# Kernel optimization log

Hardware: AMD Instinct MI355X
Metric: run time of the kernel (lower is better)

## Reference

```python
import jax, jax.numpy as jnp
import numpy as np

D_MODEL = 512
N_HEADS = 8
EDGE_FEAT_DIM = 4
NUM_GRAPHS = 64
NODES_PER_GRAPH = 128
N_NODES = NUM_GRAPHS * NODES_PER_GRAPH          # 8192
EDGES_PER_GRAPH = 4096                           # avg degree 32
N_EDGES = NUM_GRAPHS * EDGES_PER_GRAPH           # 262144


def setup_inputs() -> dict:
    key = jax.random.key(0)
    ks = jax.random.split(key, 12)
    s = 0.02
    x = jax.random.normal(ks[0], (N_NODES, D_MODEL), jnp.float32)
    # edges constrained within their graph (block-diagonal structure)
    g_of_e = jnp.arange(N_EDGES, dtype=jnp.int32) // EDGES_PER_GRAPH
    src = g_of_e * NODES_PER_GRAPH + jax.random.randint(ks[1], (N_EDGES,), 0, NODES_PER_GRAPH, jnp.int32)
    dst = g_of_e * NODES_PER_GRAPH + jax.random.randint(ks[2], (N_EDGES,), 0, NODES_PER_GRAPH, jnp.int32)
    edge_index = jnp.stack([src, dst]).astype(jnp.int32)
    edge_attr = jax.random.normal(ks[3], (N_EDGES, EDGE_FEAT_DIM), jnp.float32)
    batch = jnp.repeat(jnp.arange(NUM_GRAPHS, dtype=jnp.int32), NODES_PER_GRAPH)
    # projection weights (in,out) convention: y = x @ W + b
    Wq = jax.random.normal(ks[4], (D_MODEL, D_MODEL), jnp.float32) * s
    Wk = jax.random.normal(ks[5], (D_MODEL, D_MODEL), jnp.float32) * s
    Wv = jax.random.normal(ks[6], (D_MODEL, D_MODEL), jnp.float32) * s
    Wo = jax.random.normal(ks[7], (D_MODEL, D_MODEL), jnp.float32) * s
    bq = jnp.zeros((D_MODEL,), jnp.float32)
    bk = jnp.zeros((D_MODEL,), jnp.float32)
    bv = jnp.zeros((D_MODEL,), jnp.float32)
    bo = jnp.zeros((D_MODEL,), jnp.float32)
    # edge bias MLP: edge_feat_dim -> d_model -> n_heads
    W1 = jax.random.normal(ks[8], (EDGE_FEAT_DIM, D_MODEL), jnp.float32) * s
    b1 = jnp.zeros((D_MODEL,), jnp.float32)
    W2 = jax.random.normal(ks[9], (D_MODEL, N_HEADS), jnp.float32) * s
    b2 = jnp.zeros((N_HEADS,), jnp.float32)
    return {"x": x, "edge_index": edge_index, "edge_attr": edge_attr, "batch": batch,
            "n_g": NODES_PER_GRAPH,
            "Wq": Wq, "bq": bq, "Wk": Wk, "bk": bk, "Wv": Wv, "bv": bv,
            "Wo": Wo, "bo": bo, "W1": W1, "b1": b1, "W2": W2, "b2": b2}


def reference(x, edge_index, edge_attr, batch, n_g, Wq, bq, Wk, bk, Wv, bv, Wo, bo, W1, b1, W2, b2):
    # batch is contiguous equal-size blocks of n_g nodes per graph, so the
    # per-graph Python loop of the original collapses to a batched (G, n_g)
    # block-diagonal attention. Dropout is identity (eval / p used only in train).
    N, d_model = x.shape
    H = W2.shape[1]
    d_k = d_model // H
    G = N // n_g
    scale = 1.0 / float(np.sqrt(d_k))

    Q = (x @ Wq + bq).reshape(G, n_g, H, d_k)
    K = (x @ Wk + bk).reshape(G, n_g, H, d_k)
    V = (x @ Wv + bv).reshape(G, n_g, H, d_k)

    # (G, i, j, h) dense per-graph scores
    scores = jnp.einsum('gihd,gjhd->gijh', Q, K) * scale

    # edge bias: MLP(edge_attr) -> (E, H), scattered at (graph, local_src, local_dst)
    bias = jax.nn.relu(edge_attr @ W1 + b1) @ W2 + b2
    ge = edge_index[0] // n_g
    ls = edge_index[0] % n_g
    ld = edge_index[1] % n_g
    scores = scores.at[ge, ls, ld].add(bias)

    attn = jax.nn.softmax(scores, axis=2)  # softmax over j (keys), matches dim=1 of (i,j,h)
    out = jnp.einsum('gijh,gjhd->gihd', attn, V).reshape(N, d_model)
    return out @ Wo + bo
```

## Files before the change

### kernel.cpp

```cpp
#include <hip/hip_runtime.h>
#include <hip/hip_bf16.h>

#define E_TOTAL 262144
#define NG      128
#define GRAPHS  64
#define NHEADS  8
#define DKH     64
#define DMODEL  512
#define NNODES  8192

typedef __bf16 bf16x8 __attribute__((ext_vector_type(8)));
typedef float  f32x4  __attribute__((ext_vector_type(4)));
typedef short  s16x4  __attribute__((ext_vector_type(4)));
typedef unsigned short u16x8 __attribute__((ext_vector_type(8)));

typedef __attribute__((address_space(3))) char lds_char;
typedef const __attribute__((address_space(1))) char glb_char;

__device__ inline __hip_bfloat16 f2hbf(float f) { return __float2bfloat16(f); }
__device__ inline unsigned short f2u16(float f) {
    return __builtin_bit_cast(unsigned short, __float2bfloat16(f));
}
__device__ inline __bf16 f2bf(float f) {
    return __builtin_bit_cast(__bf16, f2u16(f));
}

__global__ __launch_bounds__(256) void prep_kernel(
    const float* __restrict__ x, __hip_bfloat16* __restrict__ xb,
    const float* __restrict__ Wq, const float* __restrict__ Wk,
    const float* __restrict__ Wv, const float* __restrict__ Wo,
    const float* __restrict__ W1, const float* __restrict__ b1,
    const float* __restrict__ W2, const float* __restrict__ b2,
    __hip_bfloat16* __restrict__ wqkvt, __hip_bfloat16* __restrict__ wot,
    __hip_bfloat16* __restrict__ w1fragt, float* __restrict__ b1f,
    __hip_bfloat16* __restrict__ w2at, float* __restrict__ b2f)
{
    int blk0 = blockIdx.x, tid = threadIdx.x;
    if (blk0 < 4096) {
        int idx = (blk0 * 256 + tid) * 4;
        float4 v = *(const float4*)(x + idx);
        ushort4 o;
        o.x = f2u16(v.x); o.y = f2u16(v.y); o.z = f2u16(v.z); o.w = f2u16(v.w);
        *(ushort4*)((unsigned short*)xb + idx) = o;
        return;
    }
    int blk = blk0 - 4096;
    if (blk < 256) {
        __shared__ __align__(16) __hip_bfloat16 tile[64][65];
        const float* src;
        __hip_bfloat16* dstT;
        int n0, k0, nb;
        if (blk < 192) {
            int nt = blk % 24, ktile = blk / 24;
            n0 = nt * 64; k0 = ktile * 64;
            if (n0 < 512)       { src = Wq; nb = n0; }
            else if (n0 < 1024) { src = Wk; nb = n0 - 512; }
            else                { src = Wv; nb = n0 - 1024; }
            dstT = wqkvt;
        } else {
            int t = blk - 192;
            n0 = (t % 8) * 64; k0 = (t / 8) * 64; nb = n0;
            src = Wo; dstT = wot;
        }
        #pragma unroll
        for (int i = 0; i < 16; ++i) {
            int idx = tid + i * 256;
            int kr = idx >> 6, nc = idx & 63;
            tile[kr][nc] = f2hbf(src[(size_t)(k0 + kr) * 512 + nb + nc]);
        }
        __syncthreads();
        #pragma unroll
        for (int i = 0; i < 16; ++i) {
            int idx = tid + i * 256;
            int nr = idx >> 6, kc = idx & 63;
            dstT[(size_t)(n0 + nr) * 512 + k0 + kc] = tile[kc][nr];
        }
    } else {
        __hip_bfloat16 z = f2hbf(0.f);
        for (int n = tid; n < 512; n += 256) {
            #pragma unroll
            for (int j = 0; j < 4; ++j) w1fragt[n * 8 + j] = f2hbf(W1[(size_t)j * 512 + n]);
            #pragma unroll
            for (int j = 4; j < 8; ++j) w1fragt[n * 8 + j] = z;
        }
        for (int i = tid; i < 512; i += 256) b1f[i] = b1[i];
        for (int i = tid; i < 32 * 64 * 4; i += 256) {
            int t = i >> 8, lane = (i >> 2) & 63, j = i & 3;
            int q = lane >> 4, l = lane & 15;
            w2at[i] = (l < 8) ? f2hbf(W2[(size_t)(16 * t + 4 * q + j) * 8 + l]) : z;
        }
        if (tid < 8) b2f[tid] = b2[tid];
    }
}

__device__ __forceinline__ void gemm_body(
    const __hip_bfloat16* __restrict__ A, const __hip_bfloat16* __restrict__ BT,
    int mode, int row0, int col0,
    const float* __restrict__ bq, const float* __restrict__ bk,
    const float* __restrict__ bv,
    __hip_bfloat16* __restrict__ qkv, __hip_bfloat16* __restrict__ vt,
    const float* __restrict__ bo, float* __restrict__ out,
    __hip_bfloat16* As, __hip_bfloat16* Bs)
{
    const int K = 512;
    int tid = threadIdx.x;
    int lane = tid & 63, quad = lane >> 4, l16 = lane & 15;
    int wave = tid >> 6, wi = wave >> 1, wj = wave & 1;

    f32x4 acc[4][4];
    #pragma unroll
    for (int a = 0; a < 4; a++)
        #pragma unroll
        for (int b = 0; b < 4; b++)
            #pragma unroll
            for (int r = 0; r < 4; r++) acc[a][b][r] = 0.f;

    const __hip_bfloat16* Ag0 = A + (size_t)(row0 + (tid >> 2)) * K + (tid & 3) * 8;
    const __hip_bfloat16* Ag1 = Ag0 + (size_t)64 * K;
    const __hip_bfloat16* Bg0 = BT + (size_t)(col0 + (tid >> 2)) * K + (tid & 3) * 8;
    const __hip_bfloat16* Bg1 = Bg0 + (size_t)64 * K;
    char* AsB = (char*)As;
    char* BsB = (char*)Bs;

    for (int kt = 0; kt < K / 32; ++kt) {
        __syncthreads();
        __builtin_amdgcn_global_load_lds((glb_char*)(Ag0 + kt * 32), (lds_char*)(AsB + tid * 16), 16, 0, 0);
        __builtin_amdgcn_global_load_lds((glb_char*)(Ag1 + kt * 32), (lds_char*)(AsB + 4096 + tid * 16), 16, 0, 0);
        __builtin_amdgcn_global_load_lds((glb_char*)(Bg0 + kt * 32), (lds_char*)(BsB + tid * 16), 16, 0, 0);
        __builtin_amdgcn_global_load_lds((glb_char*)(Bg1 + kt * 32), (lds_char*)(BsB + 4096 + tid * 16), 16, 0, 0);
        __syncthreads();
        bf16x8 af[4], bfr[4];
        #pragma unroll
        for (int t = 0; t < 4; t++)
            af[t] = *(const bf16x8*)&As[(wi * 64 + t * 16 + l16) * 32 + quad * 8];
        #pragma unroll
        for (int t = 0; t < 4; t++)
            bfr[t] = *(const bf16x8*)&Bs[(wj * 64 + t * 16 + l16) * 32 + quad * 8];
        #pragma unroll
        for (int ti = 0; ti < 4; ti++)
            #pragma unroll
            for (int tj = 0; tj < 4; tj++)
                acc[ti][tj] = __builtin_amdgcn_mfma_f32_16x16x32_bf16(af[ti], bfr[tj], acc[ti][tj], 0, 0, 0);
    }

    #pragma unroll
    for (int ti = 0; ti < 4; ti++)
        #pragma unroll
        for (int tj = 0; tj < 4; tj++) {
            int c = col0 + wj * 64 + tj * 16 + l16;
            #pragma unroll
            for (int r = 0; r < 4; r++) {
                int rw = row0 + wi * 64 + ti * 16 + quad * 4 + r;
                float v = acc[ti][tj][r];
                if (mode == 0) {
                    if (c < 1024) {
                        v += (c < 512) ? bq[c] : bk[c - 512];
                        qkv[(size_t)rw * 1536 + c] = f2hbf(v);
                    } else {
                        v += bv[c - 1024];
                        int g = rw >> 7, i = rw & 127, hh = (c - 1024) >> 6, d = (c - 1024) & 63;
                        vt[(((size_t)(g * 8 + hh)) * 64 + d) * 128 + i] = f2hbf(v);
                    }
                } else {
                    out[(size_t)rw * 512 + c] = v + bo[c];
                }
            }
        }
}

__device__ __forceinline__ void edge_body(
    int eblk,
    const float* __restrict__ ea,
    const __hip_bfloat16* __restrict__ w1fragt, const float* __restrict__ b1f,
    const __hip_bfloat16* __restrict__ w2at, const float* __restrict__ b2f,
    float* __restrict__ biasE)
{
    int tid = threadIdx.x, wave = tid >> 6, lane = tid & 63;
    int quad = lane >> 4, l16 = lane & 15;
    int eb = eblk * 256 + wave * 64;

    bf16x8 eaf[4] = {};
    if (quad == 0) {
        #pragma unroll
        for (int gg = 0; gg < 4; ++gg) {
            float4 e4 = *(const float4*)(ea + (size_t)(eb + gg * 16 + l16) * 4);
            eaf[gg][0] = f2bf(e4.x); eaf[gg][1] = f2bf(e4.y);
            eaf[gg][2] = f2bf(e4.z); eaf[gg][3] = f2bf(e4.w);
        }
    }

    f32x4 c2[4];
    #pragma unroll
    for (int gg = 0; gg < 4; ++gg)
        #pragma unroll
        for (int r = 0; r < 4; ++r) c2[gg][r] = 0.f;

    #pragma unroll 4
    for (int t = 0; t < 32; ++t) {
        bf16x8 a1 = *(const bf16x8*)(w1fragt + ((size_t)t * 16 + l16) * 8);
        float4 b14 = *(const float4*)(b1f + t * 16 + quad * 4);
        s16x4 a2 = *(const s16x4*)(w2at + ((size_t)t * 64 + lane) * 4);
        #pragma unroll
        for (int gg = 0; gg < 4; ++gg) {
            f32x4 c1 = {0.f, 0.f, 0.f, 0.f};
            c1 = __builtin_amdgcn_mfma_f32_16x16x32_bf16(a1, eaf[gg], c1, 0, 0, 0);
            s16x4 hfrag;
            hfrag[0] = (short)f2u16(fmaxf(c1[0] + b14.x, 0.f));
            hfrag[1] = (short)f2u16(fmaxf(c1[1] + b14.y, 0.f));
            hfrag[2] = (short)f2u16(fmaxf(c1[2] + b14.z, 0.f));
            hfrag[3] = (short)f2u16(fmaxf(c1[3] + b14.w, 0.f));
            c2[gg] = __builtin_amdgcn_mfma_f32_16x16x16bf16_1k(a2, hfrag, c2[gg], 0, 0, 0);
        }
    }
    if (quad < 2) {
        #pragma unroll
        for (int gg = 0; gg < 4; ++gg) {
            #pragma unroll
            for (int r = 0; r < 4; ++r) {
                int hh = quad * 4 + r;
                biasE[(size_t)hh * E_TOTAL + eb + gg * 16 + l16] = c2[gg][r] + b2f[hh];
            }
        }
    }
}

__global__ __launch_bounds__(256) void mega_kernel(
    const __hip_bfloat16* __restrict__ A, const __hip_bfloat16* __restrict__ BT,
    const float* __restrict__ bq, const float* __restrict__ bk,
    const float* __restrict__ bv,
    __hip_bfloat16* __restrict__ qkv, __hip_bfloat16* __restrict__ vt,
    const float* __restrict__ ea,
    const __hip_bfloat16* __restrict__ w1fragt, const float* __restrict__ b1f,
    const __hip_bfloat16* __restrict__ w2at, const float* __restrict__ b2f,
    float* __restrict__ biasE)
{
    __shared__ __align__(16) __hip_bfloat16 As[128 * 32];
    __shared__ __align__(16) __hip_bfloat16 Bs[128 * 32];
    int blk = blockIdx.x;
    if (blk < 768) {
        gemm_body(A, BT, 0, (blk & 63) * 128, (blk >> 6) * 128,
                  bq, bk, bv, qkv, vt, nullptr, nullptr, As, Bs);
    } else {
        edge_body(blk - 768, ea, w1fragt, b1f, w2at, b2f, biasE);
    }
}

__global__ __launch_bounds__(256) void gemm1_kernel(
    const __hip_bfloat16* __restrict__ A, const __hip_bfloat16* __restrict__ BT,
    const float* __restrict__ bo, float* __restrict__ out)
{
    __shared__ __align__(16) __hip_bfloat16 As[128 * 32];
    __shared__ __align__(16) __hip_bfloat16 Bs[128 * 32];
    gemm_body(A, BT, 1, blockIdx.x * 128, blockIdx.y * 128,
              nullptr, nullptr, nullptr, nullptr, nullptr, bo, out, As, Bs);
}

#define SS 132
__global__ __launch_bounds__(256) void attn_kernel(
    const __hip_bfloat16* __restrict__ qkv,
    const __hip_bfloat16* __restrict__ vt,
    const float* __restrict__ biasE,
    const int* __restrict__ eidx,
    __hip_bfloat16* __restrict__ O)
{
    __shared__ __align__(16) float S[128 * SS];
    int blk = blockIdx.x, g = blk & 63, h = blk >> 6;
    int tid = threadIdx.x, wave = tid >> 6, lane = tid & 63;
    int quad = lane >> 4, l16 = lane & 15;

    int   sa[16];
    float bv[16];
    #pragma unroll
    for (int u = 0; u < 16; ++u) {
        int idx = g * 4096 + tid + u * 256;
        int ls = eidx[idx] & 127;
        int ld = eidx[E_TOTAL + idx] & 127;
        sa[u] = ls * SS + ld;
        bv[u] = biasE[(size_t)h * E_TOTAL + idx];
    }

    const __hip_bfloat16* qbase = qkv + (size_t)(g * 128) * 1536 + h * 64;
    const __hip_bfloat16* kbase = qbase + 512;

    f32x4 acc[2][8];
    #pragma unroll
    for (int t = 0; t < 2; t++)
        #pragma unroll
        for (int j = 0; j < 8; j++)
            #pragma unroll
            for (int r = 0; r < 4; r++) acc[t][j][r] = 0.f;

    #pragma unroll
    for (int k0 = 0; k0 < 64; k0 += 32) {
        bf16x8 af[2];
        #pragma unroll
        for (int t = 0; t < 2; t++) {
            int m = wave * 32 + t * 16 + l16;
            af[t] = *(const bf16x8*)(qbase + (size_t)m * 1536 + k0 + quad * 8);
        }
        #pragma unroll
        for (int tj = 0; tj < 8; tj++) {
            int n = tj * 16 + l16;
            bf16x8 bfr = *(const bf16x8*)(kbase + (size_t)n * 1536 + k0 + quad * 8);
            #pragma unroll
            for (int t = 0; t < 2; t++)
                acc[t][tj] = __builtin_amdgcn_mfma_f32_16x16x32_bf16(af[t], bfr, acc[t][tj], 0, 0, 0);
        }
    }
    #pragma unroll
    for (int t = 0; t < 2; t++)
        #pragma unroll
        for (int tj = 0; tj < 8; tj++)
            #pragma unroll
            for (int r = 0; r < 4; r++) {
                int i = wave * 32 + t * 16 + quad * 4 + r;
                int j = tj * 16 + l16;
                S[i * SS + j] = acc[t][tj][r] * 0.125f;
            }
    __syncthreads();

    #pragma unroll
    for (int u = 0; u < 16; ++u)
        atomicAdd(&S[sa[u]], bv[u]);
    __syncthreads();

    #pragma unroll 4
    for (int r = wave * 32; r < wave * 32 + 32; ++r) {
        float2 v = *(const float2*)&S[r * SS + 2 * lane];
        float m = fmaxf(v.x, v.y);
        #pragma unroll
        for (int off = 32; off > 0; off >>= 1) m = fmaxf(m, __shfl_xor(m, off));
        float e0 = __expf(v.x - m), e1 = __expf(v.y - m);
        float s = e0 + e1;
        #pragma unroll
        for (int off = 32; off > 0; off >>= 1) s += __shfl_xor(s, off);
        float inv = 1.0f / s;
        float2 o; o.x = e0 * inv; o.y = e1 * inv;
        *(float2*)&S[r * SS + 2 * lane] = o;
    }
    __syncthreads();

    f32x4 oacc[2][4];
    #pragma unroll
    for (int t = 0; t < 2; t++)
        #pragma unroll
        for (int j = 0; j < 4; j++)
            #pragma unroll
            for (int r = 0; r < 4; r++) oacc[t][j][r] = 0.f;

    const __hip_bfloat16* vbase = vt + (size_t)(g * 8 + h) * 64 * 128;
    #pragma unroll
    for (int k0 = 0; k0 < 128; k0 += 32) {
        bf16x8 af[2];
        #pragma unroll
        for (int t = 0; t < 2; t++) {
            int m = wave * 32 + t * 16 + l16;
            const float* p = &S[m * SS + k0 + quad * 8];
            f32x4 xa = *(const f32x4*)p;
            f32x4 xb = *(const f32x4*)(p + 4);
            bf16x8 a;
            a[0] = f2bf(xa[0]); a[1] = f2bf(xa[1]); a[2] = f2bf(xa[2]); a[3] = f2bf(xa[3]);
            a[4] = f2bf(xb[0]); a[5] = f2bf(xb[1]); a[6] = f2bf(xb[2]); a[7] = f2bf(xb[3]);
            af[t] = a;
        }
        #pragma unroll
        for (int tj = 0; tj < 4; tj++) {
            int d = tj * 16 + l16;
            bf16x8 bfr = *(const bf16x8*)(vbase + (size_t)d * 128 + k0 + quad * 8);
            #pragma unroll
            for (int t = 0; t < 2; t++)
                oacc[t][tj] = __builtin_amdgcn_mfma_f32_16x16x32_bf16(af[t], bfr, oacc[t][tj], 0, 0, 0);
        }
    }
    #pragma unroll
    for (int t = 0; t < 2; t++)
        #pragma unroll
        for (int tj = 0; tj < 4; tj++)
            #pragma unroll
            for (int r = 0; r < 4; r++) {
                int i = wave * 32 + t * 16 + quad * 4 + r;
                int d = tj * 16 + l16;
                O[(size_t)(g * 128 + i) * 512 + h * 64 + d] = f2hbf(oacc[t][tj][r]);
            }
}

#define WS_WQKVT 0x0
#define WS_WOT   0x180000
#define WS_W1FR  0x200000
#define WS_B1F   0x202000
#define WS_W2AT  0x202800
#define WS_B2F   0x206800
#define WS_XB    0x210000
#define WS_QKV   0xA10000
#define WS_VT    0x2210000
#define WS_BIASE 0x2A10000
#define WS_O     0x3210000

extern "C" void kernel_launch(void* const* d_in, const int* in_sizes, int n_in,
                              void* d_out, int out_size, void* d_ws, size_t ws_size,
                              hipStream_t stream) {
    const float* x    = (const float*)d_in[0];
    const int*   eidx = (const int*)d_in[1];
    const float* ea   = (const float*)d_in[2];
    const float* Wq = (const float*)d_in[5];
    const float* bq = (const float*)d_in[6];
    const float* Wk = (const float*)d_in[7];
    const float* bk = (const float*)d_in[8];
    const float* Wv = (const float*)d_in[9];
    const float* bv = (const float*)d_in[10];
    const float* Wo = (const float*)d_in[11];
    const float* bo = (const float*)d_in[12];
    const float* W1 = (const float*)d_in[13];
    const float* b1 = (const float*)d_in[14];
    const float* W2 = (const float*)d_in[15];
    const float* b2 = (const float*)d_in[16];

    char* ws = (char*)d_ws;
    __hip_bfloat16* wqkvt   = (__hip_bfloat16*)(ws + WS_WQKVT);
    __hip_bfloat16* wot     = (__hip_bfloat16*)(ws + WS_WOT);
    __hip_bfloat16* w1fragt = (__hip_bfloat16*)(ws + WS_W1FR);
    float* b1f   = (float*)(ws + WS_B1F);
    __hip_bfloat16* w2at    = (__hip_bfloat16*)(ws + WS_W2AT);
    float* b2f   = (float*)(ws + WS_B2F);
    __hip_bfloat16* xb  = (__hip_bfloat16*)(ws + WS_XB);
    __hip_bfloat16* qkv = (__hip_bfloat16*)(ws + WS_QKV);
    __hip_bfloat16* vt  = (__hip_bfloat16*)(ws + WS_VT);
    float* biasE = (float*)(ws + WS_BIASE);
    __hip_bfloat16* O   = (__hip_bfloat16*)(ws + WS_O);

    prep_kernel<<<4096 + 257, 256, 0, stream>>>(x, xb, Wq, Wk, Wv, Wo, W1, b1, W2, b2,
                                                wqkvt, wot, w1fragt, b1f, w2at, b2f);
    mega_kernel<<<768 + E_TOTAL / 256, 256, 0, stream>>>(
        xb, wqkvt, bq, bk, bv, qkv, vt,
        ea, w1fragt, b1f, w2at, b2f, biasE);
    attn_kernel<<<GRAPHS * NHEADS, 256, 0, stream>>>(qkv, vt, biasE, eidx, O);
    gemm1_kernel<<<dim3(NNODES / 128, 512 / 128), 256, 0, stream>>>(
        O, wot, bo, (float*)d_out);
}
```

Baseline: 217.9 us.

## Split attention blocks by query-row halves to double grid size

Each attention block now handles 64 query rows of one (graph, head) pair instead of 128, doubling the grid to 1024 blocks and halving the LDS score buffer. Edge bias entries whose source node falls in the other half are skipped. This raises occupancy and spreads work over more CUs (512 blocks versus 256 CUs before). In exchange, both blocks of a pair read all edge indices and biases, plus K and V, so that global traffic is duplicated.

```diff
diff --git a/kernel.cpp b/kernel.cpp
--- a/kernel.cpp
+++ b/kernel.cpp
@@ -263,8 +263,10 @@
     const int* __restrict__ eidx,
     __hip_bfloat16* __restrict__ O)
 {
-    __shared__ __align__(16) float S[128 * SS];
-    int blk = blockIdx.x, g = blk & 63, h = blk >> 6;
+    __shared__ __align__(16) float S[64 * SS];
+    int blk = blockIdx.x, g = blk & 63, hh = blk >> 6;
+    int h = hh >> 1, half = hh & 1;
+    int i0 = half * 64;
     int tid = threadIdx.x, wave = tid >> 6, lane = tid & 63;
     int quad = lane >> 4, l16 = lane & 15;
 
@@ -275,57 +277,47 @@
         int idx = g * 4096 + tid + u * 256;
         int ls = eidx[idx] & 127;
         int ld = eidx[E_TOTAL + idx] & 127;
-        sa[u] = ls * SS + ld;
+        sa[u] = ((ls >> 6) == half) ? (ls & 63) * SS + ld : -1;
         bv[u] = biasE[(size_t)h * E_TOTAL + idx];
     }
 
-    const __hip_bfloat16* qbase = qkv + (size_t)(g * 128) * 1536 + h * 64;
-    const __hip_bfloat16* kbase = qbase + 512;
-
-    f32x4 acc[2][8];
-    #pragma unroll
-    for (int t = 0; t < 2; t++)
-        #pragma unroll
-        for (int j = 0; j < 8; j++)
-            #pragma unroll
-            for (int r = 0; r < 4; r++) acc[t][j][r] = 0.f;
+    const __hip_bfloat16* qbase = qkv + (size_t)(g * 128 + i0) * 1536 + h * 64;
+    const __hip_bfloat16* kbase = qkv + (size_t)(g * 128) * 1536 + h * 64 + 512;
+
+    f32x4 acc[8];
+    #pragma unroll
+    for (int j = 0; j < 8; j++)
+        #pragma unroll
+        for (int r = 0; r < 4; r++) acc[j][r] = 0.f;
 
     #pragma unroll
     for (int k0 = 0; k0 < 64; k0 += 32) {
-        bf16x8 af[2];
-        #pragma unroll
-        for (int t = 0; t < 2; t++) {
-            int m = wave * 32 + t * 16 + l16;
-            af[t] = *(const bf16x8*)(qbase + (size_t)m * 1536 + k0 + quad * 8);
-        }
+        int m = wave * 16 + l16;
+        bf16x8 af = *(const bf16x8*)(qbase + (size_t)m * 1536 + k0 + quad * 8);
         #pragma unroll
         for (int tj = 0; tj < 8; tj++) {
             int n = tj * 16 + l16;
             bf16x8 bfr = *(const bf16x8*)(kbase + (size_t)n * 1536 + k0 + quad * 8);
-            #pragma unroll
-            for (int t = 0; t < 2; t++)
-                acc[t][tj] = __builtin_amdgcn_mfma_f32_16x16x32_bf16(af[t], bfr, acc[t][tj], 0, 0, 0);
-        }
-    }
-    #pragma unroll
-    for (int t = 0; t < 2; t++)
-        #pragma unroll
-        for (int tj = 0; tj < 8; tj++)
-            #pragma unroll
-            for (int r = 0; r < 4; r++) {
-                int i = wave * 32 + t * 16 + quad * 4 + r;
-                int j = tj * 16 + l16;
-                S[i * SS + j] = acc[t][tj][r] * 0.125f;
-            }
+            acc[tj] = __builtin_amdgcn_mfma_f32_16x16x32_bf16(af, bfr, acc[tj], 0, 0, 0);
+        }
+    }
+    #pragma unroll
+    for (int tj = 0; tj < 8; tj++)
+        #pragma unroll
+        for (int r = 0; r < 4; r++) {
+            int i = wave * 16 + quad * 4 + r;
+            int j = tj * 16 + l16;
+            S[i * SS + j] = acc[tj][r] * 0.125f;
+        }
     __syncthreads();
 
     #pragma unroll
     for (int u = 0; u < 16; ++u)
-        atomicAdd(&S[sa[u]], bv[u]);
+        if (sa[u] >= 0) atomicAdd(&S[sa[u]], bv[u]);
     __syncthreads();
 
     #pragma unroll 4
-    for (int r = wave * 32; r < wave * 32 + 32; ++r) {
+    for (int r = wave * 16; r < wave * 16 + 16; ++r) {
         float2 v = *(const float2*)&S[r * SS + 2 * lane];
         float m = fmaxf(v.x, v.y);
         #pragma unroll
@@ -340,48 +332,37 @@
     }
     __syncthreads();
 
-    f32x4 oacc[2][4];
-    #pragma unroll
-    for (int t = 0; t < 2; t++)
-        #pragma unroll
-        for (int j = 0; j < 4; j++)
-            #pragma unroll
-            for (int r = 0; r < 4; r++) oacc[t][j][r] = 0.f;
+    f32x4 oacc[4];
+    #pragma unroll
+    for (int j = 0; j < 4; j++)
+        #pragma unroll
+        for (int r = 0; r < 4; r++) oacc[j][r] = 0.f;
 
     const __hip_bfloat16* vbase = vt + (size_t)(g * 8 + h) * 64 * 128;
     #pragma unroll
     for (int k0 = 0; k0 < 128; k0 += 32) {
-        bf16x8 af[2];
-        #pragma unroll
-        for (int t = 0; t < 2; t++) {
-            int m = wave * 32 + t * 16 + l16;
-            const float* p = &S[m * SS + k0 + quad * 8];
-            f32x4 xa = *(const f32x4*)p;
-            f32x4 xb = *(const f32x4*)(p + 4);
-            bf16x8 a;
-            a[0] = f2bf(xa[0]); a[1] = f2bf(xa[1]); a[2] = f2bf(xa[2]); a[3] = f2bf(xa[3]);
-            a[4] = f2bf(xb[0]); a[5] = f2bf(xb[1]); a[6] = f2bf(xb[2]); a[7] = f2bf(xb[3]);
-            af[t] = a;
-        }
+        int m = wave * 16 + l16;
+        const float* p = &S[m * SS + k0 + quad * 8];
+        f32x4 xa = *(const f32x4*)p;
+        f32x4 xb = *(const f32x4*)(p + 4);
+        bf16x8 af;
+        af[0] = f2bf(xa[0]); af[1] = f2bf(xa[1]); af[2] = f2bf(xa[2]); af[3] = f2bf(xa[3]);
+        af[4] = f2bf(xb[0]); af[5] = f2bf(xb[1]); af[6] = f2bf(xb[2]); af[7] = f2bf(xb[3]);
         #pragma unroll
         for (int tj = 0; tj < 4; tj++) {
             int d = tj * 16 + l16;
             bf16x8 bfr = *(const bf16x8*)(vbase + (size_t)d * 128 + k0 + quad * 8);
-            #pragma unroll
-            for (int t = 0; t < 2; t++)
-                oacc[t][tj] = __builtin_amdgcn_mfma_f32_16x16x32_bf16(af[t], bfr, oacc[t][tj], 0, 0, 0);
-        }
-    }
-    #pragma unroll
-    for (int t = 0; t < 2; t++)
-        #pragma unroll
-        for (int tj = 0; tj < 4; tj++)
-            #pragma unroll
-            for (int r = 0; r < 4; r++) {
-                int i = wave * 32 + t * 16 + quad * 4 + r;
-                int d = tj * 16 + l16;
-                O[(size_t)(g * 128 + i) * 512 + h * 64 + d] = f2hbf(oacc[t][tj][r]);
-            }
+            oacc[tj] = __builtin_amdgcn_mfma_f32_16x16x32_bf16(af, bfr, oacc[tj], 0, 0, 0);
+        }
+    }
+    #pragma unroll
+    for (int tj = 0; tj < 4; tj++)
+        #pragma unroll
+        for (int r = 0; r < 4; r++) {
+            int i = i0 + wave * 16 + quad * 4 + r;
+            int d = tj * 16 + l16;
+            O[(size_t)(g * 128 + i) * 512 + h * 64 + d] = f2hbf(oacc[tj][r]);
+        }
 }
 
 #define WS_WQKVT 0x0
@@ -433,7 +414,7 @@
     mega_kernel<<<768 + E_TOTAL / 256, 256, 0, stream>>>(
         xb, wqkvt, bq, bk, bv, qkv, vt,
         ea, w1fragt, b1f, w2at, b2f, biasE);
-    attn_kernel<<<GRAPHS * NHEADS, 256, 0, stream>>>(qkv, vt, biasE, eidx, O);
+    attn_kernel<<<GRAPHS * NHEADS * 2, 256, 0, stream>>>(qkv, vt, biasE, eidx, O);
     gemm1_kernel<<<dim3(NNODES / 128, 512 / 128), 256, 0, stream>>>(
         O, wot, bo, (float*)d_out);
 }
```

Result: slower. 223.2 us (+2.4%).
